# Optimization experiments

Hardware: AMD Instinct MI355X
Metric: run time of the kernel (lower is better)

The kernel has to match this reference:

```python
import jax, jax.numpy as jnp
import numpy as np
import math

BS = 8  # JPEG block size
QUALITY = 250.0  # __scale_quality(20) = 5000/20
OFFSET = 128.0 / 255.0


def _dctmtx(bs=BS):
    m = np.empty((bs, bs), dtype=np.float32)
    for j in range(bs):
        for i in range(bs):
            if i == 0:
                m[i, j] = 1.0 / math.sqrt(bs)
            else:
                m[i, j] = math.sqrt(2.0 / bs) * math.cos(math.pi * (2 * j + 1) * i / (2 * bs))
    return jnp.asarray(m)


XFORM = jnp.array([[0.299, 0.587, 0.114],
                   [-0.168735892, -0.331264108, 0.5],
                   [0.5, -0.418687589, -0.081312411]], dtype=jnp.float32)


def setup_inputs() -> dict:
    key = jax.random.key(0)
    k1, k2 = jax.random.split(key)
    rgb = jax.random.uniform(k1, (16, 3, 512, 512), dtype=jnp.float32)
    # qtable: round(abs(t)+0.5)/255 -> positive integers / 255
    quantize = jax.random.randint(k2, (3, BS, BS), 1, 100).astype(jnp.float32) / 255.0
    return {"rgb": rgb, "quantize": quantize}


def _blockify(x, bs=BS):
    # x: [B, H, W] -> [B, H//bs, W//bs, bs, bs]
    b, h, w = x.shape
    return x.reshape(b, h // bs, bs, w // bs, bs).transpose(0, 1, 3, 2, 4)


def reference(rgb, quantize):
    B, C, H, W = rgb.shape
    dct = _dctmtx()
    # RGB -> YCbCr (BHWC matmul with xform^T, expressed on BCHW via einsum)
    ycbcr = jnp.einsum('bchw,kc->bkhw', rgb, XFORM)
    shift = jnp.array([0.0, OFFSET, OFFSET], dtype=rgb.dtype)[None, :, None, None]
    ycbcr = jnp.clip(ycbcr + shift, 0.0, 1.0) - OFFSET
    # chroma 2x2 mean subsample
    y = ycbcr[:, 0]                                            # [B, H, W]
    cbcr = ycbcr[:, 1:].reshape(B, 2, H // 2, 2, W // 2, 2).mean(axis=(3, 5))
    channels = [y, cbcr[:, 0], cbcr[:, 1]]
    outs = []
    for i, ch in enumerate(channels):
        blocks = _blockify(ch)                                 # [B, nh, nw, 8, 8]
        dcts = jnp.einsum('ij,bhwjk,lk->bhwil', dct, blocks, dct)
        denom = quantize[i] * (QUALITY / 100.0) + 0.5 / 255.0  # [8, 8]
        comp = jnp.round(dcts / denom)
        outs.append(comp.reshape(-1, BS, BS))
    return tuple(outs)
```

## Files before the change

### kernel.cpp

```cpp
#include <hip/hip_runtime.h>
#include <math.h>


static __device__ __forceinline__ float clip01(float v) {
    return fminf(fmaxf(v, 0.0f), 1.0f);
}

__global__ __launch_bounds__(256)
void jpeg_kernel(const float* __restrict__ rgb, const float* __restrict__ quant,
                 float* __restrict__ out)
{
    __shared__ __align__(16) float smem[4384];
    constexpr int YT  = 0;
    constexpr int CBF = 1152;
    constexpr int CRF = 2304;
    constexpr int CB8 = 3456;
    constexpr int CR8 = 3744;
    constexpr int DM  = 4032;
    constexpr int TMP = 4096;

    const int t = threadIdx.x;

    if (t < 64) {
        const int i = t >> 3, j = t & 7;
        double v;
        if (i == 0) v = 0.35355339059327373;
        else        v = 0.5 * cos(3.141592653589793 * (double)(2 * j + 1) * (double)i / 16.0);
        smem[DM + t] = (float)v;
    }

    const int wg   = blockIdx.x;
    const int b    = wg >> 8;
    const int tile = wg & 255;
    const int th   = tile >> 4;
    const int tw   = tile & 15;

    {
        const int row = t >> 3;
        const int c4  = (t & 7) << 2;
        const float* p = rgb + ((size_t)b * 3) * 262144 + (size_t)(th * 32 + row) * 512 + (tw * 32 + c4);
        const float4 R  = *(const float4*)p;
        const float4 G  = *(const float4*)(p + 262144);
        const float4 Bv = *(const float4*)(p + 524288);
        const float OFF = (float)(128.0 / 255.0);
        const float rr[4] = {R.x, R.y, R.z, R.w};
        const float gg[4] = {G.x, G.y, G.z, G.w};
        const float bb[4] = {Bv.x, Bv.y, Bv.z, Bv.w};
        float yv[4], cbv[4], crv[4];
        #pragma unroll
        for (int k = 0; k < 4; ++k) {
            const float r_ = rr[k], g_ = gg[k], b_ = bb[k];
            const float y  = (float)(0.299) * r_ + (float)(0.587) * g_ + (float)(0.114) * b_;
            const float cb = (float)(-0.168735892) * r_ + (float)(-0.331264108) * g_ + 0.5f * b_;
            const float cr = 0.5f * r_ + (float)(-0.418687589) * g_ + (float)(-0.081312411) * b_;
            yv[k]  = clip01(y) - OFF;
            cbv[k] = clip01(cb + OFF);
            crv[k] = clip01(cr + OFF);
        }
        *(float4*)&smem[YT  + row * 36 + c4] = make_float4(yv[0], yv[1], yv[2], yv[3]);
        *(float4*)&smem[CBF + row * 36 + c4] = make_float4(cbv[0], cbv[1], cbv[2], cbv[3]);
        *(float4*)&smem[CRF + row * 36 + c4] = make_float4(crv[0], crv[1], crv[2], crv[3]);
    }
    __syncthreads();

    {
        const float OFF = (float)(128.0 / 255.0);
        const int pr = t >> 4, pc = t & 15;
        const int o00 = (2 * pr) * 36 + 2 * pc;
        const int o10 = o00 + 36;
        float sb = smem[CBF + o00];
        sb = sb + smem[CBF + o00 + 1];
        sb = sb + smem[CBF + o10];
        sb = sb + smem[CBF + o10 + 1];
        smem[CB8 + pr * 18 + pc] = sb * 0.25f - OFF;
        const float cr_r0 = smem[CRF + o00] + smem[CRF + o00 + 1];
        const float cr_r1 = smem[CRF + o10] + smem[CRF + o10 + 1];
        smem[CR8 + pr * 18 + pc] = (cr_r0 + cr_r1) * 0.25f - OFF;
    }
    __syncthreads();

    const int g = t >> 6;
    const int r = (t >> 3) & 7;
    const int c = t & 7;
    float Dr[8], Dc[8];
    #pragma unroll
    for (int k = 0; k < 8; ++k) { Dr[k] = smem[DM + r * 8 + k]; Dc[k] = smem[DM + c * 8 + k]; }
    const int qi = r * 8 + c;
    const float qadd = (float)(0.5 / 255.0);
    const float den0 = __fadd_rn(__fmul_rn(quant[qi],        2.5f), qadd);
    const float den1 = __fadd_rn(__fmul_rn(quant[64 + qi],   2.5f), qadd);
    const float den2 = __fadd_rn(__fmul_rn(quant[128 + qi],  2.5f), qadd);

    #pragma unroll
    for (int it = 0; it < 6; ++it) {
        const int sb = it * 4 + g;
        int xoff, ldx; size_t oidx; float den;
        if (sb < 16) {
            const int sr = sb >> 2, sc = sb & 3;
            xoff = YT + sr * 8 * 36 + sc * 8; ldx = 36;
            const int bh = th * 4 + sr, bw = tw * 4 + sc;
            oidx = (((size_t)(b * 64 + bh)) * 64 + bw) * 64 + (r * 8 + c);
            den = den0;
        } else if (sb < 20) {
            const int s = sb - 16, sr = s >> 1, sc = s & 1;
            xoff = CB8 + sr * 8 * 18 + sc * 8; ldx = 18;
            const int bh = th * 2 + sr, bw = tw * 2 + sc;
            oidx = (size_t)4194304 + (((size_t)(b * 32 + bh)) * 32 + bw) * 64 + (r * 8 + c);
            den = den1;
        } else {
            const int s = sb - 20, sr = s >> 1, sc = s & 1;
            xoff = CR8 + sr * 8 * 18 + sc * 8; ldx = 18;
            const int bh = th * 2 + sr, bw = tw * 2 + sc;
            oidx = (size_t)5242880 + (((size_t)(b * 32 + bh)) * 32 + bw) * 64 + (r * 8 + c);
            den = den2;
        }
        float s1 = 0.0f;
        #pragma unroll
        for (int j = 0; j < 8; ++j) s1 += Dr[j] * smem[xoff + j * ldx + c];
        smem[TMP + g * 72 + r * 9 + c] = s1;
        float s2 = 0.0f;
        #pragma unroll
        for (int k = 0; k < 8; ++k) s2 += smem[TMP + g * 72 + r * 9 + k] * Dc[k];
        out[oidx] = rintf(s2 / den);
    }
}

extern "C" void kernel_launch(void* const* d_in, const int* in_sizes, int n_in,
                              void* d_out, int out_size, void* d_ws, size_t ws_size,
                              hipStream_t stream) {
    const float* rgb   = (const float*)d_in[0];
    const float* quant = (const float*)d_in[1];
    float* out = (float*)d_out;
    dim3 grid(4096), block(256);
    hipLaunchKernelGGL(jpeg_kernel, grid, block, 0, stream, rgb, quant, out);
}
```

Measured before the change: 21.15 us.

## Restructure DCT stage: per-thread block rows, constant DCT matrix, vectorized stores

Changes the DCT phase so each lane holds one column of one 8x8 block. It runs the row pass against a compile-time DCT matrix, writes the intermediate to LDS, then reads one row back with float4 loads for the column pass. Output goes out as two float4 stores per lane instead of scalar strided stores. The quant table is staged in LDS, and the intermediate buffer reuses the dead full-resolution chroma region. This cuts LDS traffic and global store instructions. In exchange, 16 of every 64 lanes sit idle, and the write/read of the temp buffer relies on lockstep within a wavefront with no barrier.

```diff
diff --git a/kernel.cpp b/kernel.cpp
--- a/kernel.cpp
+++ b/kernel.cpp
@@ -6,28 +6,41 @@
     return fminf(fmaxf(v, 0.0f), 1.0f);
 }
 
+#define M1f 0.49039264020161522f
+#define M2f 0.46193976625564337f
+#define M3f 0.41573480615127262f
+#define M4f 0.35355339059327376f
+#define M5f 0.27778511650980111f
+#define M6f 0.19134171618254489f
+#define M7f 0.097545161008064134f
+
+static constexpr float Dm[8][8] = {
+    { M4f,  M4f,  M4f,  M4f,  M4f,  M4f,  M4f,  M4f},
+    { M1f,  M3f,  M5f,  M7f, -M7f, -M5f, -M3f, -M1f},
+    { M2f,  M6f, -M6f, -M2f, -M2f, -M6f,  M6f,  M2f},
+    { M3f, -M7f, -M1f, -M5f,  M5f,  M1f,  M7f, -M3f},
+    { M4f, -M4f, -M4f,  M4f,  M4f, -M4f, -M4f,  M4f},
+    { M5f, -M1f,  M7f,  M3f, -M3f, -M7f,  M1f, -M5f},
+    { M6f, -M2f,  M2f, -M6f, -M6f,  M2f, -M2f,  M6f},
+    { M7f, -M5f,  M3f, -M1f,  M1f, -M3f,  M5f, -M7f},
+};
+
 __global__ __launch_bounds__(256)
 void jpeg_kernel(const float* __restrict__ rgb, const float* __restrict__ quant,
                  float* __restrict__ out)
 {
-    __shared__ __align__(16) float smem[4384];
+    __shared__ __align__(16) float smem[4224];
     constexpr int YT  = 0;
     constexpr int CBF = 1152;
     constexpr int CRF = 2304;
+    constexpr int TMP = 1152;
     constexpr int CB8 = 3456;
     constexpr int CR8 = 3744;
-    constexpr int DM  = 4032;
-    constexpr int TMP = 4096;
+    constexpr int QNT = 4032;
 
     const int t = threadIdx.x;
 
-    if (t < 64) {
-        const int i = t >> 3, j = t & 7;
-        double v;
-        if (i == 0) v = 0.35355339059327373;
-        else        v = 0.5 * cos(3.141592653589793 * (double)(2 * j + 1) * (double)i / 16.0);
-        smem[DM + t] = (float)v;
-    }
+    if (t < 192) smem[QNT + t] = quant[t];
 
     const int wg   = blockIdx.x;
     const int b    = wg >> 8;
@@ -79,49 +92,59 @@
     }
     __syncthreads();
 
-    const int g = t >> 6;
-    const int r = (t >> 3) & 7;
-    const int c = t & 7;
-    float Dr[8], Dc[8];
-    #pragma unroll
-    for (int k = 0; k < 8; ++k) { Dr[k] = smem[DM + r * 8 + k]; Dc[k] = smem[DM + c * 8 + k]; }
-    const int qi = r * 8 + c;
-    const float qadd = (float)(0.5 / 255.0);
-    const float den0 = __fadd_rn(__fmul_rn(quant[qi],        2.5f), qadd);
-    const float den1 = __fadd_rn(__fmul_rn(quant[64 + qi],   2.5f), qadd);
-    const float den2 = __fadd_rn(__fmul_rn(quant[128 + qi],  2.5f), qadd);
+    const int w  = t >> 6;
+    const int l  = t & 63;
+    const int bi = l >> 3;
+    const int lc = l & 7;
 
-    #pragma unroll
-    for (int it = 0; it < 6; ++it) {
-        const int sb = it * 4 + g;
-        int xoff, ldx; size_t oidx; float den;
+    if (bi < 6) {
+        const int sb = w * 6 + bi;
+        int xoff, ldx, ch; size_t obase;
         if (sb < 16) {
             const int sr = sb >> 2, sc = sb & 3;
-            xoff = YT + sr * 8 * 36 + sc * 8; ldx = 36;
-            const int bh = th * 4 + sr, bw = tw * 4 + sc;
-            oidx = (((size_t)(b * 64 + bh)) * 64 + bw) * 64 + (r * 8 + c);
-            den = den0;
+            xoff = YT + sr * 288 + sc * 8; ldx = 36; ch = 0;
+            obase = (((size_t)(b * 64 + th * 4 + sr)) * 64 + (tw * 4 + sc)) * 64;
         } else if (sb < 20) {
             const int s = sb - 16, sr = s >> 1, sc = s & 1;
-            xoff = CB8 + sr * 8 * 18 + sc * 8; ldx = 18;
-            const int bh = th * 2 + sr, bw = tw * 2 + sc;
-            oidx = (size_t)4194304 + (((size_t)(b * 32 + bh)) * 32 + bw) * 64 + (r * 8 + c);
-            den = den1;
+            xoff = CB8 + sr * 144 + sc * 8; ldx = 18; ch = 1;
+            obase = (size_t)4194304 + (((size_t)(b * 32 + th * 2 + sr)) * 32 + (tw * 2 + sc)) * 64;
         } else {
             const int s = sb - 20, sr = s >> 1, sc = s & 1;
-            xoff = CR8 + sr * 8 * 18 + sc * 8; ldx = 18;
-            const int bh = th * 2 + sr, bw = tw * 2 + sc;
-            oidx = (size_t)5242880 + (((size_t)(b * 32 + bh)) * 32 + bw) * 64 + (r * 8 + c);
-            den = den2;
+            xoff = CR8 + sr * 144 + sc * 8; ldx = 18; ch = 2;
+            obase = (size_t)5242880 + (((size_t)(b * 32 + th * 2 + sr)) * 32 + (tw * 2 + sc)) * 64;
         }
-        float s1 = 0.0f;
+
+        float x[8];
         #pragma unroll
-        for (int j = 0; j < 8; ++j) s1 += Dr[j] * smem[xoff + j * ldx + c];
-        smem[TMP + g * 72 + r * 9 + c] = s1;
-        float s2 = 0.0f;
+        for (int j = 0; j < 8; ++j) x[j] = smem[xoff + j * ldx + lc];
+        const int tbase = TMP + w * 408 + bi * 68;
         #pragma unroll
-        for (int k = 0; k < 8; ++k) s2 += smem[TMP + g * 72 + r * 9 + k] * Dc[k];
-        out[oidx] = rintf(s2 / den);
+        for (int i = 0; i < 8; ++i) {
+            float s = 0.0f;
+            #pragma unroll
+            for (int j = 0; j < 8; ++j) s += Dm[i][j] * x[j];
+            smem[tbase + i * 8 + lc] = s;
+        }
+
+        float tr[8], q[8];
+        *(float4*)&tr[0] = *(const float4*)&smem[tbase + lc * 8];
+        *(float4*)&tr[4] = *(const float4*)&smem[tbase + lc * 8 + 4];
+        *(float4*)&q[0]  = *(const float4*)&smem[QNT + ch * 64 + lc * 8];
+        *(float4*)&q[4]  = *(const float4*)&smem[QNT + ch * 64 + lc * 8 + 4];
+
+        const float qadd = (float)(0.5 / 255.0);
+        float o[8];
+        #pragma unroll
+        for (int cc = 0; cc < 8; ++cc) {
+            float s = 0.0f;
+            #pragma unroll
+            for (int k = 0; k < 8; ++k) s += tr[k] * Dm[cc][k];
+            const float den = __fadd_rn(__fmul_rn(q[cc], 2.5f), qadd);
+            o[cc] = rintf(s / den);
+        }
+        float* op = out + obase + lc * 8;
+        *(float4*)&op[0] = make_float4(o[0], o[1], o[2], o[3]);
+        *(float4*)&op[4] = make_float4(o[4], o[5], o[6], o[7]);
     }
 }
 
```

Result: faster. 18.05 us (-14.6%).
